# Performance work log

Measured on AMD Instinct MI355X. Metric: run time of the kernel, lower is better.

Reference implementation:

```python
import jax, jax.numpy as jnp
import numpy as np

N, F, D, C, K, E, M = 50000, 512, 128, 128, 3, 20000, 8  # nodes, feat, emb, conv, cheb K, hyperedges, edge size
EPS = 1e-5


def setup_inputs() -> dict:
    key = jax.random.key(0)
    ks = jax.random.split(key, 9)
    pos_set = jax.random.normal(ks[0], (N, F), jnp.float32)
    # each hyperedge = M distinct nodes (contiguous window => distinct, like the original expansion assumes)
    base = jax.random.randint(ks[1], (E, 1), 0, N - M)
    members = (base + jnp.arange(M, dtype=jnp.int32)[None, :]).astype(jnp.int32)  # [E, M]
    # expansion(): full directed clique (no self loops) on the E*M duplicated entries
    row, col = np.where(~np.eye(M, dtype=bool))            # M*(M-1) intra-edge pairs
    offs = np.arange(E, dtype=np.int64)[:, None] * M
    edge_index = jnp.asarray(np.stack([(offs + row[None, :]).ravel(),
                                       (offs + col[None, :]).ravel()]), jnp.int32)  # [2, E*M*(M-1)]
    batch = jnp.asarray(np.repeat(np.arange(E, dtype=np.int64), M), jnp.int32)      # [E*M]
    W_enc = jax.random.normal(ks[2], (F, D), jnp.float32) / np.float32(np.sqrt(F))
    b_enc = jnp.zeros((D,), jnp.float32)
    gn_gamma = 1.0 + 0.1 * jax.random.normal(ks[3], (D,), jnp.float32)
    gn_beta = 0.01 * jax.random.normal(ks[4], (D,), jnp.float32)
    gn_alpha = 1.0 + 0.1 * jax.random.normal(ks[5], (D,), jnp.float32)
    cheb_W = jax.random.normal(ks[6], (K, D, C), jnp.float32) / np.float32(np.sqrt(D * K))
    cheb_b = jnp.zeros((C,), jnp.float32)
    lin_W = jax.random.normal(ks[7], (2 * C, 1), jnp.float32) / np.float32(np.sqrt(2 * C))
    lin_b = jnp.zeros((1,), jnp.float32)
    return dict(pos_set=pos_set, W_enc=W_enc, b_enc=b_enc, gn_gamma=gn_gamma, gn_beta=gn_beta,
                gn_alpha=gn_alpha, cheb_W=cheb_W, cheb_b=cheb_b, lin_W=lin_W, lin_b=lin_b,
                members=members, edge_index=edge_index, batch=batch)


def reference(pos_set, W_enc, b_enc, gn_gamma, gn_beta, gn_alpha, cheb_W, cheb_b,
              lin_W, lin_b, members, edge_index, batch):
    num_entries = E * M
    # running_type == 'structure': Hardtanh(Linear(feature))
    x = jnp.clip(pos_set @ W_enc + b_enc, -1.0, 1.0)                    # [N, D]
    # partition(): duplicate node features per (node, hyperedge) incidence
    xe = x[members.reshape(-1)]                                         # [E*M, D]
    # GraphNorm (per-hyperedge group): out = gamma*(x - alpha*mean)/sqrt(var+eps) + beta
    cnt = jax.ops.segment_sum(jnp.ones((num_entries,), xe.dtype), batch, num_segments=E)  # [E]
    mean = jax.ops.segment_sum(xe, batch, num_segments=E) / cnt[:, None]
    ctr = xe - gn_alpha * mean[batch]
    var = jax.ops.segment_sum(ctr * ctr, batch, num_segments=E) / cnt[:, None]
    xe = gn_gamma * ctr / jnp.sqrt(var + EPS)[batch] + gn_beta
    # AlphaDropout is identity at eval time
    # ChebConv: sym norm, lambda_max=2 => L_hat = -D^{-1/2} A D^{-1/2} (zero diagonal)
    src, dst = edge_index[0], edge_index[1]
    deg = jax.ops.segment_sum(jnp.ones_like(src, dtype=xe.dtype), dst, num_segments=num_entries)
    w = -jax.lax.rsqrt(deg[src] * deg[dst])                             # [nE] scaled-Laplacian weights

    def Lhat(h):  # sparse matvec via gather + segment scatter-add
        return jax.ops.segment_sum(w[:, None] * h[src], dst, num_segments=num_entries)

    Tx0 = xe
    Tx1 = Lhat(Tx0)
    out = Tx0 @ cheb_W[0] + Tx1 @ cheb_W[1]
    Tkm1, Tkm2 = Tx1, Tx0
    for k in range(2, K):  # K is a small static constant
        Tk = 2.0 * Lhat(Tkm1) - Tkm2
        out = out + Tk @ cheb_W[k]
        Tkm1, Tkm2 = Tk, Tkm1
    h = jnp.clip(out + cheb_b, -1.0, 1.0)                               # Hardtanh
    # poolings per hyperedge
    y_max = jax.ops.segment_max(h, batch, num_segments=E)
    y_min = jax.ops.segment_min(h, batch, num_segments=E)
    y_norm = jnp.sqrt(jax.ops.segment_sum(h * h, batch, num_segments=E) / cnt[:, None])
    y = jnp.concatenate([y_max - y_min, y_norm], axis=1)                # [E, 2C]
    logits = y @ lin_W + lin_b
    return jax.nn.sigmoid(logits).squeeze(-1)                           # [E] link probabilities
```

## Files before the change

### kernel.cpp

```cpp
#include <hip/hip_runtime.h>
#include <hip/hip_bf16.h>

#define NN   50000
#define FF   512
#define DD   128
#define CC   128
#define EE   20000
#define MM   8
#define EPSV 1e-5f

typedef __attribute__((ext_vector_type(8))) short bfrag;
typedef __attribute__((ext_vector_type(4))) float f32x4;

__device__ __forceinline__ unsigned short f2bf(float f) {
    unsigned u = __builtin_bit_cast(unsigned, f);
    unsigned r = u + 0x7FFFu + ((u >> 16) & 1u);
    return (unsigned short)(r >> 16);
}
__device__ __forceinline__ float bf2f(unsigned short h) {
    unsigned u = ((unsigned)h) << 16;
    return __builtin_bit_cast(float, u);
}
__device__ __forceinline__ void split1(float a, short& hi, short& lo) {
    unsigned short h = f2bf(a);
    hi = (short)h;
    lo = (short)f2bf(a - bf2f(h));
}

__global__ void prep_kernel(const float* __restrict__ W_enc,
                            const float* __restrict__ cheb_W,
                            unsigned short* __restrict__ WencT_hi,
                            unsigned short* __restrict__ WencT_lo,
                            unsigned short* __restrict__ WabT_hi,
                            unsigned short* __restrict__ WabT_lo) {
    int tid = blockIdx.x * blockDim.x + threadIdx.x;
    int stride = gridDim.x * blockDim.x;
    for (int idx = tid; idx < DD * FF; idx += stride) {
        int n = idx / FF, k = idx % FF;
        float v = W_enc[k * DD + n];
        short hi, lo; split1(v, hi, lo);
        WencT_hi[idx] = (unsigned short)hi;
        WencT_lo[idx] = (unsigned short)lo;
    }
    const float c1 = 1.0f / 7.0f;
    const float c2 = -47.0f / 49.0f;
    const float c3 = -1.0f / 7.0f;
    const float c4 = 12.0f / 49.0f;
    for (int idx = tid; idx < DD * 256; idx += stride) {
        int c = idx / 256, k = idx % 256;
        float v;
        if (k < DD) {
            v = cheb_W[0 * DD * CC + k * CC + c]
              + c1 * cheb_W[1 * DD * CC + k * CC + c]
              + c2 * cheb_W[2 * DD * CC + k * CC + c];
        } else {
            int d = k - DD;
            v = c3 * cheb_W[1 * DD * CC + d * CC + c]
              + c4 * cheb_W[2 * DD * CC + d * CC + c];
        }
        short hi, lo; split1(v, hi, lo);
        WabT_hi[idx] = (unsigned short)hi;
        WabT_lo[idx] = (unsigned short)lo;
    }
}

__global__ __launch_bounds__(512, 4) void enc_kernel(
        const float* __restrict__ pos,
        const unsigned short* __restrict__ BT_hi,
        const unsigned short* __restrict__ BT_lo,
        const float* __restrict__ b_enc,
        float* __restrict__ x) {
    __shared__ unsigned short bsh[2][DD * 128];
    const int t = threadIdx.x;
    const int w = t >> 6, l = t & 63, l15 = l & 15, lg = l >> 4;

    const int arow = blockIdx.x * 128 + w * 16 + l15;
    const long arow_c = (arow < NN) ? (long)arow : 0;
    const float* aBase = pos + arow_c * FF + lg * 8;

    f32x4 acc[8];
#pragma unroll
    for (int i = 0; i < 8; i++) acc[i] = (f32x4){0.f, 0.f, 0.f, 0.f};

    for (int ph = 0; ph < 4; ph++) {
        if (ph) __syncthreads();
        for (int c = t; c < 4096; c += 512) {
            const int arr = c >> 11, rc = c & 2047, row = rc >> 4, slot = rc & 15;
            const unsigned short* src = (arr ? BT_lo : BT_hi) + row * FF + ph * 128 + slot * 8;
            *(bfrag*)&bsh[arr][row * 128 + ((slot ^ (row & 7)) << 3)] = *(const bfrag*)src;
        }
        __syncthreads();
#pragma unroll
        for (int ks = 0; ks < 4; ks++) {
            const float* ap = aBase + ph * 128 + ks * 32;
            const float4 a0 = *(const float4*)ap;
            const float4 a1 = *(const float4*)(ap + 4);
            const float av[8] = {a0.x, a0.y, a0.z, a0.w, a1.x, a1.y, a1.z, a1.w};
            bfrag ahi, alo;
#pragma unroll
            for (int j = 0; j < 8; j++) { short h, lo2; split1(av[j], h, lo2); ahi[j] = h; alo[j] = lo2; }
            const int sb = ks * 4 + lg;
#pragma unroll
            for (int nt = 0; nt < 8; nt++) {
                const int row = nt * 16 + l15;
                const int off = row * 128 + ((sb ^ (row & 7)) << 3);
                const bfrag bhi = *(const bfrag*)&bsh[0][off];
                const bfrag blo = *(const bfrag*)&bsh[1][off];
                acc[nt] = __builtin_amdgcn_mfma_f32_16x16x32_bf16(ahi, bhi, acc[nt], 0, 0, 0);
                acc[nt] = __builtin_amdgcn_mfma_f32_16x16x32_bf16(ahi, blo, acc[nt], 0, 0, 0);
                acc[nt] = __builtin_amdgcn_mfma_f32_16x16x32_bf16(alo, bhi, acc[nt], 0, 0, 0);
            }
        }
    }

#pragma unroll
    for (int nt = 0; nt < 8; nt++) {
        const int col = nt * 16 + l15;
        const float bias = b_enc[col];
#pragma unroll
        for (int q = 0; q < 4; q++) {
            const int r = blockIdx.x * 128 + w * 16 + lg * 4 + q;
            if (r < NN) {
                float v = acc[nt][q] + bias;
                x[(long)r * DD + col] = fminf(1.0f, fmaxf(-1.0f, v));
            }
        }
    }
}

__global__ __launch_bounds__(1024, 4) void edge_kernel(
        const float* __restrict__ x,
        const int* __restrict__ members,
        const unsigned short* __restrict__ WabT_hi,
        const unsigned short* __restrict__ WabT_lo,
        const float* __restrict__ gn_gamma,
        const float* __restrict__ gn_beta,
        const float* __restrict__ gn_alpha,
        const float* __restrict__ cheb_b,
        const float* __restrict__ lin_W,
        const float* __restrict__ lin_b,
        float* __restrict__ out) {
    __shared__ unsigned short bsh[2][DD * 256];

    const int t = threadIdx.x;
    const int w = t >> 6, l = t & 63, l15 = l & 15, lg = l >> 4;
    const int e0 = blockIdx.x * 32;

    for (int c = t; c < 8192; c += 1024) {
        const int arr = c >> 12, rc = c & 4095, row = rc >> 5, slot = rc & 31;
        const unsigned short* src = (arr ? WabT_lo : WabT_hi) + row * 256 + slot * 8;
        *(bfrag*)&bsh[arr][row * 256 + ((slot ^ (row & 7)) << 3)] = *(const bfrag*)src;
    }

    const int e = e0 + w * 2 + (l15 >> 3);
    const int node = members[e * MM + (l15 & 7)];
    const float* xrow = x + (long)node * DD + lg * 8;

    __syncthreads();

    f32x4 acc[8];
#pragma unroll
    for (int i = 0; i < 8; i++) acc[i] = (f32x4){0.f, 0.f, 0.f, 0.f};
    bfrag shi[4], slo[4];

#pragma unroll
    for (int ks = 0; ks < 4; ks++) {
        const float4 a0 = *(const float4*)(xrow + ks * 32);
        const float4 a1 = *(const float4*)(xrow + ks * 32 + 4);
        float v[8] = {a0.x, a0.y, a0.z, a0.w, a1.x, a1.y, a1.z, a1.w};
        float s[8];
#pragma unroll
        for (int j = 0; j < 8; j++) s[j] = v[j];
#pragma unroll
        for (int mk = 1; mk <= 4; mk <<= 1)
#pragma unroll
            for (int j = 0; j < 8; j++) s[j] += __shfl_xor(s[j], mk);

        const int d0 = ks * 32 + lg * 8;
        {
            const float4 al0 = *(const float4*)(gn_alpha + d0);
            const float4 al1 = *(const float4*)(gn_alpha + d0 + 4);
            const float al[8] = {al0.x, al0.y, al0.z, al0.w, al1.x, al1.y, al1.z, al1.w};
#pragma unroll
            for (int j = 0; j < 8; j++) {
                const float m = s[j] * 0.125f;
                v[j] = v[j] - al[j] * m;
                s[j] = m * (1.0f - al[j]);
            }
        }
        float t2[8];
#pragma unroll
        for (int j = 0; j < 8; j++) t2[j] = v[j] * v[j];
#pragma unroll
        for (int mk = 1; mk <= 4; mk <<= 1)
#pragma unroll
            for (int j = 0; j < 8; j++) t2[j] += __shfl_xor(t2[j], mk);

        bfrag ahi, alo2;
        {
            const float4 g0 = *(const float4*)(gn_gamma + d0);
            const float4 g1 = *(const float4*)(gn_gamma + d0 + 4);
            const float4 b0 = *(const float4*)(gn_beta + d0);
            const float4 b1 = *(const float4*)(gn_beta + d0 + 4);
            const float gm[8] = {g0.x, g0.y, g0.z, g0.w, g1.x, g1.y, g1.z, g1.w};
            const float bt[8] = {b0.x, b0.y, b0.z, b0.w, b1.x, b1.y, b1.z, b1.w};
#pragma unroll
            for (int j = 0; j < 8; j++) {
                const float sc = gm[j] * rsqrtf(t2[j] * 0.125f + EPSV);
                const float nv = sc * v[j] + bt[j];
                short h, lo2; split1(nv, h, lo2);
                ahi[j] = h; alo2[j] = lo2;
                const float S = 8.0f * (sc * s[j] + bt[j]);
                short sh, sl; split1(S, sh, sl);
                shi[ks][j] = sh; slo[ks][j] = sl;
            }
        }

        const int sb = ks * 4 + lg;
#pragma unroll
        for (int nt = 0; nt < 8; nt++) {
            const int row = nt * 16 + l15;
            const int off = row * 256 + ((sb ^ (row & 7)) << 3);
            const bfrag bhi = *(const bfrag*)&bsh[0][off];
            const bfrag blo = *(const bfrag*)&bsh[1][off];
            acc[nt] = __builtin_amdgcn_mfma_f32_16x16x32_bf16(ahi, bhi, acc[nt], 0, 0, 0);
            acc[nt] = __builtin_amdgcn_mfma_f32_16x16x32_bf16(ahi, blo, acc[nt], 0, 0, 0);
            acc[nt] = __builtin_amdgcn_mfma_f32_16x16x32_bf16(alo2, bhi, acc[nt], 0, 0, 0);
        }
    }

#pragma unroll
    for (int ks = 4; ks < 8; ks++) {
        const bfrag ahi = shi[ks - 4];
        const bfrag alo2 = slo[ks - 4];
        const int sb = ks * 4 + lg;
#pragma unroll
        for (int nt = 0; nt < 8; nt++) {
            const int row = nt * 16 + l15;
            const int off = row * 256 + ((sb ^ (row & 7)) << 3);
            const bfrag bhi = *(const bfrag*)&bsh[0][off];
            const bfrag blo = *(const bfrag*)&bsh[1][off];
            acc[nt] = __builtin_amdgcn_mfma_f32_16x16x32_bf16(ahi, bhi, acc[nt], 0, 0, 0);
            acc[nt] = __builtin_amdgcn_mfma_f32_16x16x32_bf16(ahi, blo, acc[nt], 0, 0, 0);
            acc[nt] = __builtin_amdgcn_mfma_f32_16x16x32_bf16(alo2, bhi, acc[nt], 0, 0, 0);
        }
    }

    float partial = 0.f;
#pragma unroll
    for (int nt = 0; nt < 8; nt++) {
        const int col = nt * 16 + l15;
        const float bias = cheb_b[col];
        float mx = -2.f, mn = 2.f, ssq = 0.f;
#pragma unroll
        for (int q = 0; q < 4; q++) {
            float h = acc[nt][q] + bias;
            h = fminf(1.0f, fmaxf(-1.0f, h));
            mx = fmaxf(mx, h); mn = fminf(mn, h); ssq += h * h;
        }
        mx = fmaxf(mx, __shfl_xor(mx, 16));
        mn = fminf(mn, __shfl_xor(mn, 16));
        ssq += __shfl_xor(ssq, 16);
        partial += (mx - mn) * lin_W[col] + sqrtf(ssq * 0.125f) * lin_W[DD + col];
    }
    if (lg & 1) partial = 0.f;
    partial += __shfl_xor(partial, 1);
    partial += __shfl_xor(partial, 2);
    partial += __shfl_xor(partial, 4);
    partial += __shfl_xor(partial, 8);
    if (l == 0 || l == 32) {
        const float z = partial + lin_b[0];
        out[e0 + w * 2 + (l >> 5)] = 1.0f / (1.0f + expf(-z));
    }
}

extern "C" void kernel_launch(void* const* d_in, const int* in_sizes, int n_in,
                              void* d_out, int out_size, void* d_ws, size_t ws_size,
                              hipStream_t stream) {
    const float* pos    = (const float*)d_in[0];
    const float* W_enc  = (const float*)d_in[1];
    const float* b_enc  = (const float*)d_in[2];
    const float* gammaP = (const float*)d_in[3];
    const float* betaP  = (const float*)d_in[4];
    const float* alphaP = (const float*)d_in[5];
    const float* cheb_W = (const float*)d_in[6];
    const float* cheb_b = (const float*)d_in[7];
    const float* lin_W  = (const float*)d_in[8];
    const float* lin_b  = (const float*)d_in[9];
    const int*   members = (const int*)d_in[10];
    float* out = (float*)d_out;

    char* ws = (char*)d_ws;
    float* x = (float*)ws;
    unsigned short* WencT_hi = (unsigned short*)(ws + 25600000);
    unsigned short* WencT_lo = WencT_hi + DD * FF;
    unsigned short* WabT_hi  = WencT_lo + DD * FF;
    unsigned short* WabT_lo  = WabT_hi + DD * 256;

    prep_kernel<<<256, 256, 0, stream>>>(W_enc, cheb_W, WencT_hi, WencT_lo, WabT_hi, WabT_lo);
    enc_kernel<<<(NN + 127) / 128, 512, 0, stream>>>(pos, WencT_hi, WencT_lo, b_enc, x);
    edge_kernel<<<EE / 32, 1024, 0, stream>>>(x, members, WabT_hi, WabT_lo,
                                              gammaP, betaP, alphaP, cheb_b, lin_W, lin_b, out);
}
```

Before: 266.5 us.

## Switch encoder and edge GEMMs to 32x32 MFMA with retiled LDS staging

Both kernels move from 16x16x32 to 32x32x16 bf16 MFMA tiles. The encoder now stages split hi/lo A tiles in LDS with 64-row blocks, 8 K-phases and higher occupancy. The edge kernel halves its block size, keeps only the hi weights in LDS and reads the lo weights from global memory. It also drops the lo part of the mean-sum term, computing that product with a single hi-only MFMA. This aims to raise MFMA throughput and cut LDS footprint, but gives up a little precision on the mean term and adds global weight loads inside the inner loop.

```diff
diff --git a/kernel.cpp b/kernel.cpp
--- a/kernel.cpp
+++ b/kernel.cpp
@@ -9,8 +9,10 @@
 #define MM   8
 #define EPSV 1e-5f
 
-typedef __attribute__((ext_vector_type(8))) short bfrag;
-typedef __attribute__((ext_vector_type(4))) float f32x4;
+typedef __attribute__((ext_vector_type(8)))  short bfrag;
+typedef __attribute__((ext_vector_type(16))) float f32x16;
+
+#define MFMA32(a, b, c) __builtin_amdgcn_mfma_f32_32x32x16_bf16((a), (b), (c), 0, 0, 0)
 
 __device__ __forceinline__ unsigned short f2bf(float f) {
     unsigned u = __builtin_bit_cast(unsigned, f);
@@ -64,71 +66,79 @@
     }
 }
 
-__global__ __launch_bounds__(512, 4) void enc_kernel(
+__global__ __launch_bounds__(512, 6) void enc_kernel(
         const float* __restrict__ pos,
         const unsigned short* __restrict__ BT_hi,
         const unsigned short* __restrict__ BT_lo,
         const float* __restrict__ b_enc,
         float* __restrict__ x) {
-    __shared__ unsigned short bsh[2][DD * 128];
+    __shared__ unsigned short ahz[2][64 * 64];
+    __shared__ unsigned short bhz[2][128 * 64];
+
     const int t = threadIdx.x;
-    const int w = t >> 6, l = t & 63, l15 = l & 15, lg = l >> 4;
-
-    const int arow = blockIdx.x * 128 + w * 16 + l15;
-    const long arow_c = (arow < NN) ? (long)arow : 0;
-    const float* aBase = pos + arow_c * FF + lg * 8;
-
-    f32x4 acc[8];
-#pragma unroll
-    for (int i = 0; i < 8; i++) acc[i] = (f32x4){0.f, 0.f, 0.f, 0.f};
-
-    for (int ph = 0; ph < 4; ph++) {
+    const int w = t >> 6, l = t & 63, l31 = l & 31, lg2 = l >> 5;
+    const int wm = w & 1, wn = w >> 1;
+
+    f32x16 acc;
+#pragma unroll
+    for (int i = 0; i < 16; i++) acc[i] = 0.f;
+
+    for (int ph = 0; ph < 8; ph++) {
         if (ph) __syncthreads();
-        for (int c = t; c < 4096; c += 512) {
-            const int arr = c >> 11, rc = c & 2047, row = rc >> 4, slot = rc & 15;
-            const unsigned short* src = (arr ? BT_lo : BT_hi) + row * FF + ph * 128 + slot * 8;
-            *(bfrag*)&bsh[arr][row * 128 + ((slot ^ (row & 7)) << 3)] = *(const bfrag*)src;
+        {
+            const int r = t >> 3, c8 = t & 7;
+            int grow = blockIdx.x * 64 + r;
+            if (grow >= NN) grow = NN - 1;
+            const float* src = pos + (size_t)grow * FF + ph * 64 + c8 * 8;
+            const float4 v0 = *(const float4*)src;
+            const float4 v1 = *(const float4*)(src + 4);
+            const float av[8] = {v0.x, v0.y, v0.z, v0.w, v1.x, v1.y, v1.z, v1.w};
+            bfrag hi, lo;
+#pragma unroll
+            for (int j = 0; j < 8; j++) { short h, lo2; split1(av[j], h, lo2); hi[j] = h; lo[j] = lo2; }
+            const int dst = r * 64 + ((c8 ^ (r & 7)) << 3);
+            *(bfrag*)&ahz[0][dst] = hi;
+            *(bfrag*)&ahz[1][dst] = lo;
+        }
+#pragma unroll
+        for (int i = 0; i < 4; i++) {
+            const int c = t + i * 512;
+            const int arr = c >> 10, rc = c & 1023, n = rc >> 3, slot = rc & 7;
+            const unsigned short* src = (arr ? BT_lo : BT_hi) + (size_t)n * FF + ph * 64 + slot * 8;
+            *(bfrag*)&bhz[arr][n * 64 + ((slot ^ (n & 7)) << 3)] = *(const bfrag*)src;
         }
         __syncthreads();
 #pragma unroll
         for (int ks = 0; ks < 4; ks++) {
-            const float* ap = aBase + ph * 128 + ks * 32;
-            const float4 a0 = *(const float4*)ap;
-            const float4 a1 = *(const float4*)(ap + 4);
-            const float av[8] = {a0.x, a0.y, a0.z, a0.w, a1.x, a1.y, a1.z, a1.w};
-            bfrag ahi, alo;
-#pragma unroll
-            for (int j = 0; j < 8; j++) { short h, lo2; split1(av[j], h, lo2); ahi[j] = h; alo[j] = lo2; }
-            const int sb = ks * 4 + lg;
-#pragma unroll
-            for (int nt = 0; nt < 8; nt++) {
-                const int row = nt * 16 + l15;
-                const int off = row * 128 + ((sb ^ (row & 7)) << 3);
-                const bfrag bhi = *(const bfrag*)&bsh[0][off];
-                const bfrag blo = *(const bfrag*)&bsh[1][off];
-                acc[nt] = __builtin_amdgcn_mfma_f32_16x16x32_bf16(ahi, bhi, acc[nt], 0, 0, 0);
-                acc[nt] = __builtin_amdgcn_mfma_f32_16x16x32_bf16(ahi, blo, acc[nt], 0, 0, 0);
-                acc[nt] = __builtin_amdgcn_mfma_f32_16x16x32_bf16(alo, bhi, acc[nt], 0, 0, 0);
-            }
-        }
-    }
-
-#pragma unroll
-    for (int nt = 0; nt < 8; nt++) {
-        const int col = nt * 16 + l15;
-        const float bias = b_enc[col];
-#pragma unroll
-        for (int q = 0; q < 4; q++) {
-            const int r = blockIdx.x * 128 + w * 16 + lg * 4 + q;
-            if (r < NN) {
-                float v = acc[nt][q] + bias;
-                x[(long)r * DD + col] = fminf(1.0f, fmaxf(-1.0f, v));
-            }
-        }
-    }
-}
-
-__global__ __launch_bounds__(1024, 4) void edge_kernel(
+            const int slot = ks * 2 + lg2;
+            const int arow = wm * 32 + l31;
+            const int aoff = arow * 64 + ((slot ^ (arow & 7)) << 3);
+            const bfrag ahi = *(const bfrag*)&ahz[0][aoff];
+            const bfrag alo = *(const bfrag*)&ahz[1][aoff];
+            const int col = wn * 32 + l31;
+            const int boff = col * 64 + ((slot ^ (col & 7)) << 3);
+            const bfrag bhi = *(const bfrag*)&bhz[0][boff];
+            const bfrag blo = *(const bfrag*)&bhz[1][boff];
+            acc = MFMA32(ahi, bhi, acc);
+            acc = MFMA32(ahi, blo, acc);
+            acc = MFMA32(alo, bhi, acc);
+        }
+    }
+
+    const int col = wn * 32 + l31;
+    const float bias = b_enc[col];
+    const int brow = blockIdx.x * 64 + wm * 32;
+#pragma unroll
+    for (int r = 0; r < 16; r++) {
+        const int row = brow + (r & 3) + 8 * (r >> 2) + 4 * lg2;
+        if (row < NN) {
+            float v = acc[r] + bias;
+            x[(size_t)row * DD + col] = fminf(1.0f, fmaxf(-1.0f, v));
+        }
+    }
+}
+
+__global__ __launch_bounds__(512, 4) void edge_kernel(
         const float* __restrict__ x,
         const int* __restrict__ members,
         const unsigned short* __restrict__ WabT_hi,
@@ -140,33 +150,37 @@
         const float* __restrict__ lin_W,
         const float* __restrict__ lin_b,
         float* __restrict__ out) {
-    __shared__ unsigned short bsh[2][DD * 256];
+    __shared__ unsigned short wa_hi[128 * 128];
+    __shared__ unsigned short wb_hi[128 * 128];
 
     const int t = threadIdx.x;
-    const int w = t >> 6, l = t & 63, l15 = l & 15, lg = l >> 4;
-    const int e0 = blockIdx.x * 32;
-
-    for (int c = t; c < 8192; c += 1024) {
-        const int arr = c >> 12, rc = c & 4095, row = rc >> 5, slot = rc & 31;
-        const unsigned short* src = (arr ? WabT_lo : WabT_hi) + row * 256 + slot * 8;
-        *(bfrag*)&bsh[arr][row * 256 + ((slot ^ (row & 7)) << 3)] = *(const bfrag*)src;
-    }
-
-    const int e = e0 + w * 2 + (l15 >> 3);
-    const int node = members[e * MM + (l15 & 7)];
-    const float* xrow = x + (long)node * DD + lg * 8;
+    const int w = t >> 6, l = t & 63, l31 = l & 31, lg2 = l >> 5;
+
+#pragma unroll
+    for (int i = 0; i < 8; i++) {
+        const int c = t + i * 512;
+        const int arr = c >> 11, rc = c & 2047, col = rc >> 4, slot = rc & 15;
+        const bfrag v = *(const bfrag*)(WabT_hi + (size_t)col * 256 + arr * 128 + slot * 8);
+        unsigned short* dst = arr ? wb_hi : wa_hi;
+        *(bfrag*)&dst[col * 128 + ((slot ^ (col & 15)) << 3)] = v;
+    }
+
+    const int node = members[blockIdx.x * 256 + w * 32 + l31];
+    const float* xrow = x + (size_t)node * DD;
 
     __syncthreads();
 
-    f32x4 acc[8];
-#pragma unroll
-    for (int i = 0; i < 8; i++) acc[i] = (f32x4){0.f, 0.f, 0.f, 0.f};
-    bfrag shi[4], slo[4];
-
-#pragma unroll
-    for (int ks = 0; ks < 4; ks++) {
-        const float4 a0 = *(const float4*)(xrow + ks * 32);
-        const float4 a1 = *(const float4*)(xrow + ks * 32 + 4);
+    f32x16 acc[4];
+#pragma unroll
+    for (int nt = 0; nt < 4; nt++)
+#pragma unroll
+        for (int i = 0; i < 16; i++) acc[nt][i] = 0.f;
+
+#pragma unroll
+    for (int ks = 0; ks < 8; ks++) {
+        const int koff = ks * 16 + lg2 * 8;
+        const float4 a0 = *(const float4*)(xrow + koff);
+        const float4 a1 = *(const float4*)(xrow + koff + 4);
         float v[8] = {a0.x, a0.y, a0.z, a0.w, a1.x, a1.y, a1.z, a1.w};
         float s[8];
 #pragma unroll
@@ -176,10 +190,9 @@
 #pragma unroll
             for (int j = 0; j < 8; j++) s[j] += __shfl_xor(s[j], mk);
 
-        const int d0 = ks * 32 + lg * 8;
         {
-            const float4 al0 = *(const float4*)(gn_alpha + d0);
-            const float4 al1 = *(const float4*)(gn_alpha + d0 + 4);
+            const float4 al0 = *(const float4*)(gn_alpha + koff);
+            const float4 al1 = *(const float4*)(gn_alpha + koff + 4);
             const float al[8] = {al0.x, al0.y, al0.z, al0.w, al1.x, al1.y, al1.z, al1.w};
 #pragma unroll
             for (int j = 0; j < 8; j++) {
@@ -196,12 +209,12 @@
 #pragma unroll
             for (int j = 0; j < 8; j++) t2[j] += __shfl_xor(t2[j], mk);
 
-        bfrag ahi, alo2;
+        bfrag ahi, alo, shi;
         {
-            const float4 g0 = *(const float4*)(gn_gamma + d0);
-            const float4 g1 = *(const float4*)(gn_gamma + d0 + 4);
-            const float4 b0 = *(const float4*)(gn_beta + d0);
-            const float4 b1 = *(const float4*)(gn_beta + d0 + 4);
+            const float4 g0 = *(const float4*)(gn_gamma + koff);
+            const float4 g1 = *(const float4*)(gn_gamma + koff + 4);
+            const float4 b0 = *(const float4*)(gn_beta + koff);
+            const float4 b1 = *(const float4*)(gn_beta + koff + 4);
             const float gm[8] = {g0.x, g0.y, g0.z, g0.w, g1.x, g1.y, g1.z, g1.w};
             const float bt[8] = {b0.x, b0.y, b0.z, b0.w, b1.x, b1.y, b1.z, b1.w};
 #pragma unroll
@@ -209,68 +222,59 @@
                 const float sc = gm[j] * rsqrtf(t2[j] * 0.125f + EPSV);
                 const float nv = sc * v[j] + bt[j];
                 short h, lo2; split1(nv, h, lo2);
-                ahi[j] = h; alo2[j] = lo2;
+                ahi[j] = h; alo[j] = lo2;
                 const float S = 8.0f * (sc * s[j] + bt[j]);
-                short sh, sl; split1(S, sh, sl);
-                shi[ks][j] = sh; slo[ks][j] = sl;
+                shi[j] = (short)f2bf(S);
             }
         }
 
-        const int sb = ks * 4 + lg;
-#pragma unroll
-        for (int nt = 0; nt < 8; nt++) {
-            const int row = nt * 16 + l15;
-            const int off = row * 256 + ((sb ^ (row & 7)) << 3);
-            const bfrag bhi = *(const bfrag*)&bsh[0][off];
-            const bfrag blo = *(const bfrag*)&bsh[1][off];
-            acc[nt] = __builtin_amdgcn_mfma_f32_16x16x32_bf16(ahi, bhi, acc[nt], 0, 0, 0);
-            acc[nt] = __builtin_amdgcn_mfma_f32_16x16x32_bf16(ahi, blo, acc[nt], 0, 0, 0);
-            acc[nt] = __builtin_amdgcn_mfma_f32_16x16x32_bf16(alo2, bhi, acc[nt], 0, 0, 0);
-        }
-    }
-
-#pragma unroll
-    for (int ks = 4; ks < 8; ks++) {
-        const bfrag ahi = shi[ks - 4];
-        const bfrag alo2 = slo[ks - 4];
-        const int sb = ks * 4 + lg;
-#pragma unroll
-        for (int nt = 0; nt < 8; nt++) {
-            const int row = nt * 16 + l15;
-            const int off = row * 256 + ((sb ^ (row & 7)) << 3);
-            const bfrag bhi = *(const bfrag*)&bsh[0][off];
-            const bfrag blo = *(const bfrag*)&bsh[1][off];
-            acc[nt] = __builtin_amdgcn_mfma_f32_16x16x32_bf16(ahi, bhi, acc[nt], 0, 0, 0);
-            acc[nt] = __builtin_amdgcn_mfma_f32_16x16x32_bf16(ahi, blo, acc[nt], 0, 0, 0);
-            acc[nt] = __builtin_amdgcn_mfma_f32_16x16x32_bf16(alo2, bhi, acc[nt], 0, 0, 0);
-        }
-    }
-
-    float partial = 0.f;
-#pragma unroll
-    for (int nt = 0; nt < 8; nt++) {
-        const int col = nt * 16 + l15;
+        const int slot = ks * 2 + lg2;
+#pragma unroll
+        for (int nt = 0; nt < 4; nt++) {
+            const int col = nt * 32 + l31;
+            const int woff = col * 128 + ((slot ^ (col & 15)) << 3);
+            const bfrag wahi = *(const bfrag*)&wa_hi[woff];
+            const bfrag wbh  = *(const bfrag*)&wb_hi[woff];
+            const bfrag walo = *(const bfrag*)(WabT_lo + (size_t)col * 256 + koff);
+            acc[nt] = MFMA32(ahi, wahi, acc[nt]);
+            acc[nt] = MFMA32(ahi, walo, acc[nt]);
+            acc[nt] = MFMA32(alo, wahi, acc[nt]);
+            acc[nt] = MFMA32(shi, wbh,  acc[nt]);
+        }
+    }
+
+    float p[4] = {0.f, 0.f, 0.f, 0.f};
+#pragma unroll
+    for (int nt = 0; nt < 4; nt++) {
+        const int col = nt * 32 + l31;
         const float bias = cheb_b[col];
-        float mx = -2.f, mn = 2.f, ssq = 0.f;
-#pragma unroll
-        for (int q = 0; q < 4; q++) {
-            float h = acc[nt][q] + bias;
-            h = fminf(1.0f, fmaxf(-1.0f, h));
-            mx = fmaxf(mx, h); mn = fminf(mn, h); ssq += h * h;
-        }
-        mx = fmaxf(mx, __shfl_xor(mx, 16));
-        mn = fminf(mn, __shfl_xor(mn, 16));
-        ssq += __shfl_xor(ssq, 16);
-        partial += (mx - mn) * lin_W[col] + sqrtf(ssq * 0.125f) * lin_W[DD + col];
-    }
-    if (lg & 1) partial = 0.f;
-    partial += __shfl_xor(partial, 1);
-    partial += __shfl_xor(partial, 2);
-    partial += __shfl_xor(partial, 4);
-    partial += __shfl_xor(partial, 8);
-    if (l == 0 || l == 32) {
-        const float z = partial + lin_b[0];
-        out[e0 + w * 2 + (l >> 5)] = 1.0f / (1.0f + expf(-z));
+        const float w1 = lin_W[col], w2 = lin_W[DD + col];
+#pragma unroll
+        for (int e = 0; e < 4; e++) {
+            float mx = -2.f, mn = 2.f, ssq = 0.f;
+#pragma unroll
+            for (int q = 0; q < 4; q++) {
+                float h = acc[nt][e * 4 + q] + bias;
+                h = fminf(1.0f, fmaxf(-1.0f, h));
+                mx = fmaxf(mx, h); mn = fminf(mn, h); ssq += h * h;
+            }
+            mx = fmaxf(mx, __shfl_xor(mx, 32));
+            mn = fminf(mn, __shfl_xor(mn, 32));
+            ssq += __shfl_xor(ssq, 32);
+            p[e] += (mx - mn) * w1 + sqrtf(ssq * 0.125f) * w2;
+        }
+    }
+#pragma unroll
+    for (int mk = 1; mk <= 16; mk <<= 1)
+#pragma unroll
+        for (int e = 0; e < 4; e++) p[e] += __shfl_xor(p[e], mk);
+    if (l == 0) {
+        const float b0 = lin_b[0];
+#pragma unroll
+        for (int e = 0; e < 4; e++) {
+            const float z = p[e] + b0;
+            out[blockIdx.x * 32 + w * 4 + e] = 1.0f / (1.0f + expf(-z));
+        }
     }
 }
 
@@ -298,7 +302,7 @@
     unsigned short* WabT_lo  = WabT_hi + DD * 256;
 
     prep_kernel<<<256, 256, 0, stream>>>(W_enc, cheb_W, WencT_hi, WencT_lo, WabT_hi, WabT_lo);
-    enc_kernel<<<(NN + 127) / 128, 512, 0, stream>>>(pos, WencT_hi, WencT_lo, b_enc, x);
-    edge_kernel<<<EE / 32, 1024, 0, stream>>>(x, members, WabT_hi, WabT_lo,
-                                              gammaP, betaP, alphaP, cheb_b, lin_W, lin_b, out);
-}
+    enc_kernel<<<(NN + 63) / 64, 512, 0, stream>>>(pos, WencT_hi, WencT_lo, b_enc, x);
+    edge_kernel<<<EE / 32, 512, 0, stream>>>(x, members, WabT_hi, WabT_lo,
+                                             gammaP, betaP, alphaP, cheb_b, lin_W, lin_b, out);
+}
```

Result: no change. 262.5 us (-1.5%).
